# Performance work log

Measured on AMD Instinct MI355X. Metric: run time of the kernel, lower is better.

Reference implementation:

```python
import jax, jax.numpy as jnp
import numpy as np

DIM = 768
HEADS = 12
DIM_HEAD = DIM // HEADS  # 64
INNER = DIM_HEAD * HEADS  # 768
HIDDEN = 4 * DIM  # 3072
N = 31  # num_patches + 1, fixed by Block (num_patches=30)
B = 512
EPS = 1e-5
MASK_VAL = -987654321.0


def layernorm(x, g, b):
    mu = jnp.mean(x, axis=-1, keepdims=True)
    var = jnp.mean(jnp.square(x - mu), axis=-1, keepdims=True)
    return (x - mu) * jax.lax.rsqrt(var + EPS) * g + b


def setup_inputs() -> dict:
    key = jax.random.key(0)
    ks = jax.random.split(key, 12)
    s = 0.02
    return {
        "x": jax.random.normal(ks[0], (B, N, DIM), jnp.float32),
        "ln1_g": jnp.ones((DIM,), jnp.float32),
        "ln1_b": jnp.zeros((DIM,), jnp.float32),
        "w_qkv": jax.random.normal(ks[1], (DIM, 3 * INNER), jnp.float32) * s,
        "scale": jnp.full((HEADS,), DIM_HEAD ** -0.5, jnp.float32),
        "w_o": jax.random.normal(ks[2], (INNER, DIM), jnp.float32) * s,
        "b_o": jnp.zeros((DIM,), jnp.float32),
        "ln2_g": jnp.ones((DIM,), jnp.float32),
        "ln2_b": jnp.zeros((DIM,), jnp.float32),
        "w1": jax.random.normal(ks[3], (DIM, HIDDEN), jnp.float32) * s,
        "b1": jnp.zeros((HIDDEN,), jnp.float32),
        "w2": jax.random.normal(ks[4], (HIDDEN, DIM), jnp.float32) * s,
        "b2": jnp.zeros((DIM,), jnp.float32),
    }


def reference(x, ln1_g, ln1_b, w_qkv, scale, w_o, b_o, ln2_g, ln2_b, w1, b1, w2, b2):
    b, n, _ = x.shape
    # --- LSA attention ---
    h = layernorm(x, ln1_g, ln1_b)
    qkv = h @ w_qkv  # [b, n, 3*inner]
    q, k, v = jnp.split(qkv, 3, axis=-1)
    def split_heads(t):
        return t.reshape(b, n, HEADS, DIM_HEAD).transpose(0, 2, 1, 3)  # b h n d
    q, k, v = split_heads(q), split_heads(k), split_heads(v)
    dots = jnp.einsum('bhid,bhjd->bhij', q, k) * scale[None, :, None, None]
    # diagonal exclusion mask (self-token masked out)
    diag = jnp.eye(n, dtype=bool)
    dots = jnp.where(diag[None, None], MASK_VAL, dots)
    attn = jax.nn.softmax(dots, axis=-1)
    out = jnp.einsum('bhij,bhjd->bhid', attn, v)
    out = out.transpose(0, 2, 1, 3).reshape(b, n, INNER)
    x = x + out @ w_o + b_o
    # --- MLP ---
    h2 = layernorm(x, ln2_g, ln2_b)
    h2 = jax.nn.gelu(h2 @ w1 + b1, approximate=False)
    x = x + h2 @ w2 + b2
    return x
```

## Files before the change

### kernel.cpp

```cpp
#include <hip/hip_runtime.h>
#include <math.h>

#define DIM 768
#define HEADS 12
#define DHEAD 64
#define NTOK 31
#define BATCH 512
#define MTOK (BATCH * NTOK)
#define HIDDEN 3072
#define QKVN 2304
#define MASK_VAL -987654321.0f

typedef short s16x8 __attribute__((ext_vector_type(8)));
typedef float f32x4 __attribute__((ext_vector_type(4)));

static __device__ __forceinline__ float bs2f(unsigned short u) {
  unsigned int x = ((unsigned int)u) << 16;
  return __builtin_bit_cast(float, x);
}
static __device__ __forceinline__ unsigned short f2bs(float f) {
  unsigned int x = __builtin_bit_cast(unsigned int, f);
  x += 0x7fffu + ((x >> 16) & 1u);
  return (unsigned short)(x >> 16);
}

static __device__ __forceinline__ void gload16(const unsigned short* g, unsigned short* l) {
  __builtin_amdgcn_global_load_lds(
      (const __attribute__((address_space(1))) unsigned int*)g,
      (__attribute__((address_space(3))) unsigned int*)l, 16, 0, 0);
}

static __device__ __forceinline__ float epi_apply(int EPI, float v, int col, size_t idx,
                                                  const float* bias, const void* resid) {
  if (EPI == 0) return v;
  if (EPI == 2) {
    float t = v + bias[col];
    float arg = 1.5957691216f * t * (1.f + 0.044715f * t * t);
    return t * __builtin_amdgcn_rcpf(1.f + __expf(-arg));
  }
  if (EPI == 3) return v + bias[col] + ((const float*)resid)[idx];
  return v + bias[col] + bs2f(((const unsigned short*)resid)[idx]);
}

static __device__ __forceinline__ void epi_store(int EPI, void* outp, size_t idx, float t) {
  if (EPI == 4) ((float*)outp)[idx] = t;
  else ((unsigned short*)outp)[idx] = f2bs(t);
}

__global__ __launch_bounds__(256) void transpose_kernel(const float* __restrict__ w,
                                                        unsigned short* __restrict__ wt,
                                                        int K, int N) {
  __shared__ float t[64][65];
  int k0 = blockIdx.y * 64, n0 = blockIdx.x * 64;
  int tid = threadIdx.x;
  int r = tid >> 4, c4 = (tid & 15) * 4;
#pragma unroll
  for (int i = 0; i < 4; ++i) {
    float4 v = *(const float4*)(w + (size_t)(k0 + r + i * 16) * N + n0 + c4);
    t[r + i * 16][c4] = v.x;
    t[r + i * 16][c4 + 1] = v.y;
    t[r + i * 16][c4 + 2] = v.z;
    t[r + i * 16][c4 + 3] = v.w;
  }
  __syncthreads();
#pragma unroll
  for (int i = 0; i < 4; ++i) {
    int n = r + i * 16;
    ushort4 o;
    o.x = f2bs(t[c4 + 0][n]);
    o.y = f2bs(t[c4 + 1][n]);
    o.z = f2bs(t[c4 + 2][n]);
    o.w = f2bs(t[c4 + 3][n]);
    *(ushort4*)(wt + (size_t)(n0 + n) * K + k0 + c4) = o;
  }
}

__global__ __launch_bounds__(256) void ln_kernel(const float* __restrict__ x,
                                                 const float* __restrict__ g,
                                                 const float* __restrict__ bta,
                                                 unsigned short* __restrict__ out) {
  int wid = threadIdx.x >> 6, lane = threadIdx.x & 63;
  size_t row = (size_t)blockIdx.x * 4 + wid;
  const float4* xr = (const float4*)(x + row * DIM);
  float4 v[3];
  v[0] = xr[lane];
  v[1] = xr[lane + 64];
  v[2] = xr[lane + 128];
  float s = 0.f, sq = 0.f;
#pragma unroll
  for (int i = 0; i < 3; ++i) {
    s += v[i].x + v[i].y + v[i].z + v[i].w;
    sq += v[i].x * v[i].x + v[i].y * v[i].y + v[i].z * v[i].z + v[i].w * v[i].w;
  }
#pragma unroll
  for (int off = 32; off; off >>= 1) {
    s += __shfl_xor(s, off);
    sq += __shfl_xor(sq, off);
  }
  float mu = s * (1.f / DIM);
  float var = sq * (1.f / DIM) - mu * mu;
  float rs = rsqrtf(var + 1e-5f);
#pragma unroll
  for (int i = 0; i < 3; ++i) {
    int col = i * 256 + lane * 4;
    float4 gg = *(const float4*)(g + col);
    float4 bb = *(const float4*)(bta + col);
    ushort4 o;
    o.x = f2bs((v[i].x - mu) * rs * gg.x + bb.x);
    o.y = f2bs((v[i].y - mu) * rs * gg.y + bb.y);
    o.z = f2bs((v[i].z - mu) * rs * gg.z + bb.z);
    o.w = f2bs((v[i].w - mu) * rs * gg.w + bb.w);
    *(ushort4*)(out + row * DIM + col) = o;
  }
}

__global__ __launch_bounds__(256) void ln_bf16_kernel(const unsigned short* __restrict__ x,
                                                      const float* __restrict__ g,
                                                      const float* __restrict__ bta,
                                                      unsigned short* __restrict__ out) {
  int wid = threadIdx.x >> 6, lane = threadIdx.x & 63;
  size_t row = (size_t)blockIdx.x * 4 + wid;
  const unsigned short* xr = x + row * DIM;
  float v[12];
#pragma unroll
  for (int i = 0; i < 3; ++i) {
    ushort4 u = *(const ushort4*)(xr + i * 256 + lane * 4);
    v[i * 4 + 0] = bs2f(u.x);
    v[i * 4 + 1] = bs2f(u.y);
    v[i * 4 + 2] = bs2f(u.z);
    v[i * 4 + 3] = bs2f(u.w);
  }
  float s = 0.f, sq = 0.f;
#pragma unroll
  for (int i = 0; i < 12; ++i) {
    s += v[i];
    sq += v[i] * v[i];
  }
#pragma unroll
  for (int off = 32; off; off >>= 1) {
    s += __shfl_xor(s, off);
    sq += __shfl_xor(sq, off);
  }
  float mu = s * (1.f / DIM);
  float var = sq * (1.f / DIM) - mu * mu;
  float rs = rsqrtf(var + 1e-5f);
#pragma unroll
  for (int i = 0; i < 3; ++i) {
    int col = i * 256 + lane * 4;
    float4 gg = *(const float4*)(g + col);
    float4 bb = *(const float4*)(bta + col);
    ushort4 o;
    o.x = f2bs((v[i * 4 + 0] - mu) * rs * gg.x + bb.x);
    o.y = f2bs((v[i * 4 + 1] - mu) * rs * gg.y + bb.y);
    o.z = f2bs((v[i * 4 + 2] - mu) * rs * gg.z + bb.z);
    o.w = f2bs((v[i * 4 + 3] - mu) * rs * gg.w + bb.w);
    *(ushort4*)(out + row * DIM + col) = o;
  }
}

template <int BUF, int MH, int KH, int VM, typename STF>
__device__ __forceinline__ void gphase(const char* aP0, const char* aP1,
                                       const char* bP0, const char* bP1,
                                       s16x8* bk, f32x4 (&acc)[8][4], STF&& stage) {
  const char* aP = BUF ? aP1 : aP0;
  const char* bP = BUF ? bP1 : bP0;
  s16x8 af[4];
  if (MH == 0) {
#pragma unroll
    for (int ni = 0; ni < 4; ++ni)
      bk[ni] = *(const s16x8*)(bP + KH * 16384 + ni * 1024);
  }
#pragma unroll
  for (int mi = 0; mi < 4; ++mi)
    af[mi] = *(const s16x8*)(aP + KH * 16384 + MH * 4096 + mi * 1024);
  stage();
  if (VM == 10) asm volatile("s_waitcnt vmcnt(10)");
  if (VM == 4) asm volatile("s_waitcnt vmcnt(4)");
  if (VM == 0) asm volatile("s_waitcnt vmcnt(0)");
  __builtin_amdgcn_s_barrier();
  asm volatile("s_waitcnt lgkmcnt(0)");
  __builtin_amdgcn_s_setprio(1);
#pragma unroll
  for (int mi = 0; mi < 4; ++mi)
#pragma unroll
    for (int ni = 0; ni < 4; ++ni)
      acc[MH * 4 + mi][ni] =
          __builtin_amdgcn_mfma_f32_16x16x32_bf16(af[mi], bk[ni], acc[MH * 4 + mi][ni], 0, 0, 0);
  __builtin_amdgcn_s_setprio(0);
  __builtin_amdgcn_s_barrier();
}

template <int EPI>
__device__ __forceinline__ void gemm8_body(
    const unsigned short* __restrict__ A, const unsigned short* __restrict__ Bt,
    void* __restrict__ outp, const float* __restrict__ bias,
    const void* __restrict__ resid, int M, int N, int K, int ntn) {
  __shared__ unsigned short lds[65536];
  const char* ldsb = (const char*)lds;
  int tid = threadIdx.x;
  int lane = tid & 63, w = tid >> 6;
  int wm = w >> 2, wn = w & 3;
  int fr = lane & 15, q = lane >> 4;

  int nwg = gridDim.x, orig = blockIdx.x;
  int qd = nwg >> 3, r8 = nwg & 7, xcd = orig & 7, loc = orig >> 3;
  int bid = (xcd < r8 ? xcd * (qd + 1) : r8 * (qd + 1) + (xcd - r8) * qd) + loc;
  int m0 = (bid / ntn) * 256, n0 = (bid % ntn) * 256;

  int rdoff = (q * 16) ^ (((fr >> 1) & 3) << 4);
  const char* aP0 = ldsb + (wm * 128 + fr) * 64 + rdoff;
  const char* aP1 = aP0 + 65536;
  const char* bP0 = ldsb + 32768 + (wn * 64 + fr) * 64 + rdoff;
  const char* bP1 = bP0 + 65536;

  int srow = tid >> 2;
  int seoff = (((tid & 3) ^ ((srow >> 1) & 3))) << 3;
  const char* Ab = (const char*)A + ((size_t)(m0 + srow) * K + seoff) * 2;
  const char* Bb = (const char*)Bt + ((size_t)(n0 + srow) * K + seoff) * 2;
  size_t rstep = (size_t)K * 256;

  auto stg = [&](int mat, int kh, int buf, int tile) {
    const char* gp = (mat ? Bb : Ab) + tile * 128 + kh * 64;
    unsigned short* lp = lds + buf * 32768 + mat * 16384 + kh * 8192 + w * 512;
    gload16((const unsigned short*)gp, lp);
    gload16((const unsigned short*)(gp + rstep), lp + 4096);
  };
  auto nop = [&] {};

  f32x4 acc[8][4] = {};
  s16x8 bk[4];
  int NT = K / 64;

  stg(1, 0, 0, 0);
  stg(0, 0, 0, 0);
  stg(1, 1, 0, 0);
  stg(0, 1, 0, 0);
  stg(1, 0, 1, 1);
  stg(0, 0, 1, 1);
  stg(1, 1, 1, 1);
  asm volatile("s_waitcnt vmcnt(6)");
  __builtin_amdgcn_s_barrier();

  for (int t = 0; t + 3 < NT; t += 2) {
    gphase<0, 0, 0, -1>(aP0, aP1, bP0, bP1, bk, acc, [&] { stg(0, 1, 1, t + 1); });
    gphase<0, 1, 0, 10>(aP0, aP1, bP0, bP1, bk, acc, [&] { stg(1, 0, 0, t + 2); });
    gphase<0, 0, 1, -1>(aP0, aP1, bP0, bP1, bk, acc, [&] { stg(0, 0, 0, t + 2); });
    gphase<0, 1, 1, 10>(aP0, aP1, bP0, bP1, bk, acc, [&] { stg(1, 1, 0, t + 2); });
    gphase<1, 0, 0, -1>(aP0, aP1, bP0, bP1, bk, acc, [&] { stg(0, 1, 0, t + 2); });
    gphase<1, 1, 0, 10>(aP0, aP1, bP0, bP1, bk, acc, [&] { stg(1, 0, 1, t + 3); });
    gphase<1, 0, 1, -1>(aP0, aP1, bP0, bP1, bk, acc, [&] { stg(0, 0, 1, t + 3); });
    gphase<1, 1, 1, 10>(aP0, aP1, bP0, bP1, bk, acc, [&] { stg(1, 1, 1, t + 3); });
  }
  gphase<0, 0, 0, -1>(aP0, aP1, bP0, bP1, bk, acc, [&] { stg(0, 1, 1, NT - 1); });
  gphase<0, 1, 0, -1>(aP0, aP1, bP0, bP1, bk, acc, nop);
  gphase<0, 0, 1, -1>(aP0, aP1, bP0, bP1, bk, acc, nop);
  gphase<0, 1, 1, 4>(aP0, aP1, bP0, bP1, bk, acc, nop);
  gphase<1, 0, 0, -1>(aP0, aP1, bP0, bP1, bk, acc, nop);
  gphase<1, 1, 0, 0>(aP0, aP1, bP0, bP1, bk, acc, nop);
  gphase<1, 0, 1, -1>(aP0, aP1, bP0, bP1, bk, acc, nop);
  gphase<1, 1, 1, -1>(aP0, aP1, bP0, bP1, bk, acc, nop);

#pragma unroll
  for (int am = 0; am < 8; ++am)
#pragma unroll
    for (int ni = 0; ni < 4; ++ni)
#pragma unroll
      for (int rr = 0; rr < 4; ++rr) {
        int row = m0 + wm * 128 + am * 16 + (lane >> 4) * 4 + rr;
        int col = n0 + wn * 64 + ni * 16 + fr;
        size_t idx = (size_t)row * N + col;
        epi_store(EPI, outp, idx, epi_apply(EPI, acc[am][ni][rr], col, idx, bias, resid));
      }
}

template <int BUF, int MH, int KH, int VM, typename STF>
__device__ __forceinline__ void gph192(const char* aB0, const char* bKH0, const char* bKH1,
                                       s16x8 (&bk)[3], f32x4 (&acc)[8][3], STF&& stage) {
  const char* aP = aB0 + BUF * 32768 + KH * 16384 + MH * 4096;
  s16x8 af[4];
  if (MH == 0) {
    const char* bp = (KH ? bKH1 : bKH0) + BUF * 24576;
#pragma unroll
    for (int ni = 0; ni < 3; ++ni) bk[ni] = *(const s16x8*)(bp + ni * 2048);
  }
#pragma unroll
  for (int mi = 0; mi < 4; ++mi) af[mi] = *(const s16x8*)(aP + mi * 1024);
  stage();
  if (VM == 2) asm volatile("s_waitcnt vmcnt(2)");
  if (VM == 0) asm volatile("s_waitcnt vmcnt(0)");
  __builtin_amdgcn_s_barrier();
  asm volatile("s_waitcnt lgkmcnt(0)");
  __builtin_amdgcn_s_setprio(1);
#pragma unroll
  for (int mi = 0; mi < 4; ++mi)
#pragma unroll
    for (int ni = 0; ni < 3; ++ni)
      acc[MH * 4 + mi][ni] =
          __builtin_amdgcn_mfma_f32_16x16x32_bf16(af[mi], bk[ni], acc[MH * 4 + mi][ni], 0, 0, 0);
  __builtin_amdgcn_s_setprio(0);
  __builtin_amdgcn_s_barrier();
}

template <int EPI>
__device__ __forceinline__ void gemm192_body(
    const unsigned short* __restrict__ A, const unsigned short* __restrict__ Bt,
    void* __restrict__ outp, const float* __restrict__ bias,
    const void* __restrict__ resid, int M, int N, int K, int ntn) {
  __shared__ char ldsc[114688];
  int tid = threadIdx.x;
  int lane = tid & 63, w = tid >> 6;
  int wm = w >> 2, wn = w & 3;
  int fr = lane & 15, q = lane >> 4;

  int nwg = gridDim.x, orig = blockIdx.x;
  int qd = nwg >> 3, r8 = nwg & 7, xcd = orig & 7, loc = orig >> 3;
  int bid = (xcd < r8 ? xcd * (qd + 1) : r8 * (qd + 1) + (xcd - r8) * qd) + loc;
  int m0 = (bid / ntn) * 256, n0 = (bid % ntn) * 192;

  int rdoffA = (q * 16) ^ (((fr >> 1) & 3) << 4);
  const char* aB0 = ldsc + (wm * 128 + fr) * 64 + rdoffA;
  int brow0 = wn * 48 + fr;
  int bsw = brow0 & 7;
  const char* bBase = ldsc + 65536 + brow0 * 128 + (q ^ (bsw & 3)) * 16;
  const char* bKH0 = bBase + ((0 ^ (bsw >> 2)) * 64);
  const char* bKH1 = bBase + ((1 ^ (bsw >> 2)) * 64);

  int srow = tid >> 2;
  int seoffA = (((tid & 3) ^ ((srow >> 1) & 3))) << 3;
  const char* Ab = (const char*)A + ((size_t)(m0 + srow) * K + seoffA) * 2;
  size_t rstep = (size_t)K * 256;
  auto stgA = [&](int kh, int buf, int tile) {
    const char* gp = Ab + tile * 128 + kh * 64;
    unsigned short* lp = (unsigned short*)(ldsc + buf * 32768 + kh * 16384 + w * 1024);
    gload16((const unsigned short*)gp, lp);
    gload16((const unsigned short*)(gp + rstep), (unsigned short*)((char*)lp + 8192));
  };
  const char* Bb2 = (const char*)Bt +
                    ((size_t)(n0 + (tid >> 3)) * K + (((tid & 7) ^ ((tid >> 3) & 7)) * 8)) * 2;
  auto stgB = [&](int j, int buf, int tile) {
    gload16((const unsigned short*)(Bb2 + (size_t)j * 128 * K + tile * 128),
            (unsigned short*)(ldsc + 65536 + buf * 24576 + j * 8192 + w * 1024));
  };
  auto nop = [&] {};

  f32x4 acc[8][3] = {};
  s16x8 bk[3];
  int NT = K / 64;

  stgA(0, 0, 0);
  stgA(1, 0, 0);
  stgB(0, 0, 0);
  stgB(1, 0, 0);
  stgB(2, 0, 0);
  stgA(0, 1, 1);
  asm volatile("s_waitcnt vmcnt(2)");
  __builtin_amdgcn_s_barrier();

  for (int t = 0; t + 3 < NT; t += 2) {
    gph192<0, 0, 0, -1>(aB0, bKH0, bKH1, bk, acc,
                        [&] { stgA(1, 1, t + 1); stgB(0, 1, t + 1); stgB(1, 1, t + 1); });
    gph192<0, 1, 0, -1>(aB0, bKH0, bKH1, bk, acc, [&] { stgB(2, 1, t + 1); });
    gph192<0, 0, 1, -1>(aB0, bKH0, bKH1, bk, acc, [&] { stgA(0, 0, t + 2); });
    gph192<0, 1, 1, 2>(aB0, bKH0, bKH1, bk, acc, nop);
    gph192<1, 0, 0, -1>(aB0, bKH0, bKH1, bk, acc,
                        [&] { stgA(1, 0, t + 2); stgB(0, 0, t + 2); stgB(1, 0, t + 2); });
    gph192<1, 1, 0, -1>(aB0, bKH0, bKH1, bk, acc, [&] { stgB(2, 0, t + 2); });
    gph192<1, 0, 1, -1>(aB0, bKH0, bKH1, bk, acc, [&] { stgA(0, 1, t + 3); });
    gph192<1, 1, 1, 2>(aB0, bKH0, bKH1, bk, acc, nop);
  }
  gph192<0, 0, 0, -1>(aB0, bKH0, bKH1, bk, acc,
                      [&] { stgA(1, 1, NT - 1); stgB(0, 1, NT - 1); stgB(1, 1, NT - 1); });
  gph192<0, 1, 0, -1>(aB0, bKH0, bKH1, bk, acc, [&] { stgB(2, 1, NT - 1); });
  gph192<0, 0, 1, -1>(aB0, bKH0, bKH1, bk, acc, nop);
  gph192<0, 1, 1, 0>(aB0, bKH0, bKH1, bk, acc, nop);
  gph192<1, 0, 0, -1>(aB0, bKH0, bKH1, bk, acc, nop);
  gph192<1, 1, 0, -1>(aB0, bKH0, bKH1, bk, acc, nop);
  gph192<1, 0, 1, -1>(aB0, bKH0, bKH1, bk, acc, nop);
  gph192<1, 1, 1, -1>(aB0, bKH0, bKH1, bk, acc, nop);

#pragma unroll
  for (int am = 0; am < 8; ++am)
#pragma unroll
    for (int ni = 0; ni < 3; ++ni)
#pragma unroll
      for (int rr = 0; rr < 4; ++rr) {
        int row = m0 + wm * 128 + am * 16 + q * 4 + rr;
        int col = n0 + wn * 48 + ni * 16 + fr;
        size_t idx = (size_t)row * N + col;
        epi_store(EPI, outp, idx, epi_apply(EPI, acc[am][ni][rr], col, idx, bias, resid));
      }
}

__global__ __launch_bounds__(512, 2) void gemm_qkv(const unsigned short* A,
                                                   const unsigned short* Bt, void* o,
                                                   const float* b, const void* r, int M,
                                                   int N, int K, int ntn) {
  gemm8_body<0>(A, Bt, o, b, r, M, N, K, ntn);
}
__global__ __launch_bounds__(512, 2) void gemm_mlp1(const unsigned short* A,
                                                    const unsigned short* Bt, void* o,
                                                    const float* b, const void* r, int M,
                                                    int N, int K, int ntn) {
  gemm8_body<2>(A, Bt, o, b, r, M, N, K, ntn);
}
__global__ __launch_bounds__(512, 2) void gemm_proj(const unsigned short* A,
                                                    const unsigned short* Bt, void* o,
                                                    const float* b, const void* r, int M,
                                                    int N, int K, int ntn) {
  gemm192_body<3>(A, Bt, o, b, r, M, N, K, ntn);
}
__global__ __launch_bounds__(512, 2) void gemm_mlp2(const unsigned short* A,
                                                    const unsigned short* Bt, void* o,
                                                    const float* b, const void* r, int M,
                                                    int N, int K, int ntn) {
  gemm192_body<4>(A, Bt, o, b, r, M, N, K, ntn);
}

__global__ __launch_bounds__(256) void attn_mfma_kernel(const unsigned short* __restrict__ qkv,
                                                        const float* __restrict__ scale,
                                                        unsigned short* __restrict__ ao) {
  __shared__ unsigned short Vt[4][64][40];
  __shared__ unsigned short Pl[4][32][32];
  int wid = threadIdx.x >> 6, lane = threadIdx.x & 63;
  int pair = blockIdx.x * 4 + wid;
  int b = pair / HEADS, h = pair % HEADS;
  const unsigned short* base = qkv + (size_t)b * NTOK * QKVN + h * DHEAD;
  const unsigned short* Qp = base;
  const unsigned short* Kp = base + 768;
  const unsigned short* Vp = base + 1536;

  int c = lane & 15, q = lane >> 4;
  int oct = q * 8;

  unsigned short vcol[NTOK];
#pragma unroll
  for (int j = 0; j < NTOK; ++j) vcol[j] = Vp[(size_t)j * QKVN + lane];
#pragma unroll
  for (int j = 0; j < NTOK; ++j) Vt[wid][lane][j] = vcol[j];
  Vt[wid][lane][31] = 0;

  s16x8 kf[2][2] = {{{0}}}, qf[2][2] = {{{0}}};
#pragma unroll
  for (int t = 0; t < 2; ++t) {
    int row = t * 16 + c;
    if (row < NTOK) {
#pragma unroll
      for (int s = 0; s < 2; ++s) {
        kf[t][s] = *(const s16x8*)(Kp + (size_t)row * QKVN + s * 32 + oct);
        qf[t][s] = *(const s16x8*)(Qp + (size_t)row * QKVN + s * 32 + oct);
      }
    }
  }

  f32x4 st[2][2] = {};
#pragma unroll
  for (int jt = 0; jt < 2; ++jt)
#pragma unroll
    for (int it = 0; it < 2; ++it)
#pragma unroll
      for (int s = 0; s < 2; ++s)
        st[jt][it] =
            __builtin_amdgcn_mfma_f32_16x16x32_bf16(kf[jt][s], qf[it][s], st[jt][it], 0, 0, 0);

  float scl = scale[h];
  float p[2][2][4];
#pragma unroll
  for (int it = 0; it < 2; ++it)
#pragma unroll
    for (int jt = 0; jt < 2; ++jt)
#pragma unroll
      for (int r = 0; r < 4; ++r) {
        int j = jt * 16 + 4 * q + r;
        int i = it * 16 + c;
        float v = st[jt][it][r] * scl;
        if (j == 31 || j == i) v = MASK_VAL;
        p[it][jt][r] = v;
      }
#pragma unroll
  for (int it = 0; it < 2; ++it) {
    float m = p[it][0][0];
#pragma unroll
    for (int jt = 0; jt < 2; ++jt)
#pragma unroll
      for (int r = 0; r < 4; ++r) m = fmaxf(m, p[it][jt][r]);
    m = fmaxf(m, __shfl_xor(m, 16));
    m = fmaxf(m, __shfl_xor(m, 32));
    float s = 0.f;
#pragma unroll
    for (int jt = 0; jt < 2; ++jt)
#pragma unroll
      for (int r = 0; r < 4; ++r) {
        float e = __expf(p[it][jt][r] - m);
        p[it][jt][r] = e;
        s += e;
      }
    s += __shfl_xor(s, 16);
    s += __shfl_xor(s, 32);
    float inv = __builtin_amdgcn_rcpf(s);
#pragma unroll
    for (int jt = 0; jt < 2; ++jt)
#pragma unroll
      for (int r = 0; r < 4; ++r) p[it][jt][r] *= inv;
  }
#pragma unroll
  for (int it = 0; it < 2; ++it)
#pragma unroll
    for (int jt = 0; jt < 2; ++jt) {
      unsigned int w0 =
          (unsigned int)f2bs(p[it][jt][0]) | ((unsigned int)f2bs(p[it][jt][1]) << 16);
      unsigned int w1 =
          (unsigned int)f2bs(p[it][jt][2]) | ((unsigned int)f2bs(p[it][jt][3]) << 16);
      uint2 pk = {w0, w1};
      *(uint2*)&Pl[wid][it * 16 + c][jt * 16 + 4 * q] = pk;
    }

  s16x8 pa[2];
#pragma unroll
  for (int it = 0; it < 2; ++it) pa[it] = *(const s16x8*)&Pl[wid][it * 16 + c][oct];
  f32x4 o[2][4];
#pragma unroll
  for (int it = 0; it < 2; ++it)
#pragma unroll
    for (int dt = 0; dt < 4; ++dt) {
      s16x8 vb = *(const s16x8*)&Vt[wid][dt * 16 + c][oct];
      f32x4 z = {0.f, 0.f, 0.f, 0.f};
      o[it][dt] = __builtin_amdgcn_mfma_f32_16x16x32_bf16(pa[it], vb, z, 0, 0, 0);
    }
#pragma unroll
  for (int it = 0; it < 2; ++it)
#pragma unroll
    for (int r = 0; r < 4; ++r) {
      int i = it * 16 + 4 * q + r;
      if (i < NTOK) {
        size_t rowoff = ((size_t)b * NTOK + i) * DIM + h * DHEAD;
#pragma unroll
        for (int dt = 0; dt < 4; ++dt) ao[rowoff + dt * 16 + c] = f2bs(o[it][dt][r]);
      }
    }
}

extern "C" void kernel_launch(void* const* d_in, const int* in_sizes, int n_in,
                              void* d_out, int out_size, void* d_ws, size_t ws_size,
                              hipStream_t stream) {
  (void)in_sizes; (void)n_in; (void)out_size; (void)ws_size;
  const float* x = (const float*)d_in[0];
  const float* ln1_g = (const float*)d_in[1];
  const float* ln1_b = (const float*)d_in[2];
  const float* w_qkv = (const float*)d_in[3];
  const float* scale = (const float*)d_in[4];
  const float* w_o = (const float*)d_in[5];
  const float* b_o = (const float*)d_in[6];
  const float* ln2_g = (const float*)d_in[7];
  const float* ln2_b = (const float*)d_in[8];
  const float* w1 = (const float*)d_in[9];
  const float* b1 = (const float*)d_in[10];
  const float* w2 = (const float*)d_in[11];
  const float* b2 = (const float*)d_in[12];

  char* ws = (char*)d_ws;
  unsigned short* buf1 = (unsigned short*)(ws + 0);
  unsigned short* qkv_bf = (unsigned short*)(ws + 24379392);
  unsigned short* x2 = (unsigned short*)(ws + 24379392);
  unsigned short* g_bf = (unsigned short*)(ws + 97517568);
  unsigned short* wqkvT = (unsigned short*)(ws + 195035136);
  unsigned short* woT = (unsigned short*)(ws + 198574080);
  unsigned short* w1T = (unsigned short*)(ws + 199753728);
  unsigned short* w2T = (unsigned short*)(ws + 204472320);

  transpose_kernel<<<dim3(QKVN / 64, DIM / 64), 256, 0, stream>>>(w_qkv, wqkvT, DIM, QKVN);
  transpose_kernel<<<dim3(DIM / 64, DIM / 64), 256, 0, stream>>>(w_o, woT, DIM, DIM);
  transpose_kernel<<<dim3(HIDDEN / 64, DIM / 64), 256, 0, stream>>>(w1, w1T, DIM, HIDDEN);
  transpose_kernel<<<dim3(DIM / 64, HIDDEN / 64), 256, 0, stream>>>(w2, w2T, HIDDEN, DIM);

  ln_kernel<<<MTOK / 4, 256, 0, stream>>>(x, ln1_g, ln1_b, buf1);
  gemm_qkv<<<(MTOK / 256) * (QKVN / 256), 512, 0, stream>>>(
      buf1, wqkvT, qkv_bf, nullptr, nullptr, MTOK, QKVN, DIM, QKVN / 256);
  attn_mfma_kernel<<<(BATCH * HEADS) / 4, 256, 0, stream>>>(qkv_bf, scale, buf1);
  gemm_proj<<<(MTOK / 256) * (DIM / 192), 512, 0, stream>>>(
      buf1, woT, x2, b_o, x, MTOK, DIM, DIM, DIM / 192);
  ln_bf16_kernel<<<MTOK / 4, 256, 0, stream>>>(x2, ln2_g, ln2_b, buf1);
  gemm_mlp1<<<(MTOK / 256) * (HIDDEN / 256), 512, 0, stream>>>(
      buf1, w1T, g_bf, b1, nullptr, MTOK, HIDDEN, DIM, HIDDEN / 256);
  gemm_mlp2<<<(MTOK / 256) * (DIM / 192), 512, 0, stream>>>(
      g_bf, w2T, (float*)d_out, b2, x2, MTOK, DIM, HIDDEN, DIM / 192);
}
```

Before: 330.3 us.

## Shrink QKV and MLP1 GEMM tiles to 128x256 with K-step 32

Replaces the 256x256 GEMM body used by the QKV and MLP1 projections with a 128x256 tile, a 32-wide K step and 48KB of LDS. The pipeline staging, wait counts and launch bounds (now 4 blocks per CU hint) are reworked to match, and the grids double in M. The intent is more workgroups and higher occupancy to cut tail effects and raise latency hiding, at the cost of less operand reuse per tile and more barriers per unit of K.

Result: faster. 322.7 us (-2.3%).

```diff
diff --git a/kernel.cpp b/kernel.cpp
--- a/kernel.cpp
+++ b/kernel.cpp
@@ -158,45 +158,40 @@
   }
 }
 
-template <int BUF, int MH, int KH, int VM, typename STF>
-__device__ __forceinline__ void gphase(const char* aP0, const char* aP1,
-                                       const char* bP0, const char* bP1,
-                                       s16x8* bk, f32x4 (&acc)[8][4], STF&& stage) {
-  const char* aP = BUF ? aP1 : aP0;
-  const char* bP = BUF ? bP1 : bP0;
-  s16x8 af[4];
+template <int BUF, int MH, int VM, typename STF>
+__device__ __forceinline__ void gph128(const char* aP0, const char* bP0,
+                                       s16x8 (&bk)[4], f32x4 (&acc)[4][4], STF&& stage) {
+  const char* aP = aP0 + BUF * 8192 + MH * 2048;
+  const char* bP = bP0 + BUF * 16384;
+  s16x8 af[2];
   if (MH == 0) {
 #pragma unroll
-    for (int ni = 0; ni < 4; ++ni)
-      bk[ni] = *(const s16x8*)(bP + KH * 16384 + ni * 1024);
-  }
-#pragma unroll
-  for (int mi = 0; mi < 4; ++mi)
-    af[mi] = *(const s16x8*)(aP + KH * 16384 + MH * 4096 + mi * 1024);
+    for (int ni = 0; ni < 4; ++ni) bk[ni] = *(const s16x8*)(bP + ni * 1024);
+  }
+  af[0] = *(const s16x8*)(aP);
+  af[1] = *(const s16x8*)(aP + 1024);
   stage();
-  if (VM == 10) asm volatile("s_waitcnt vmcnt(10)");
-  if (VM == 4) asm volatile("s_waitcnt vmcnt(4)");
+  if (VM == 2) asm volatile("s_waitcnt vmcnt(2)");
   if (VM == 0) asm volatile("s_waitcnt vmcnt(0)");
   __builtin_amdgcn_s_barrier();
   asm volatile("s_waitcnt lgkmcnt(0)");
   __builtin_amdgcn_s_setprio(1);
 #pragma unroll
-  for (int mi = 0; mi < 4; ++mi)
+  for (int mi = 0; mi < 2; ++mi)
 #pragma unroll
     for (int ni = 0; ni < 4; ++ni)
-      acc[MH * 4 + mi][ni] =
-          __builtin_amdgcn_mfma_f32_16x16x32_bf16(af[mi], bk[ni], acc[MH * 4 + mi][ni], 0, 0, 0);
+      acc[MH * 2 + mi][ni] =
+          __builtin_amdgcn_mfma_f32_16x16x32_bf16(af[mi], bk[ni], acc[MH * 2 + mi][ni], 0, 0, 0);
   __builtin_amdgcn_s_setprio(0);
   __builtin_amdgcn_s_barrier();
 }
 
 template <int EPI>
-__device__ __forceinline__ void gemm8_body(
+__device__ __forceinline__ void gemm128_body(
     const unsigned short* __restrict__ A, const unsigned short* __restrict__ Bt,
     void* __restrict__ outp, const float* __restrict__ bias,
     const void* __restrict__ resid, int M, int N, int K, int ntn) {
-  __shared__ unsigned short lds[65536];
-  const char* ldsb = (const char*)lds;
+  __shared__ char ldsc[49152];
   int tid = threadIdx.x;
   int lane = tid & 63, w = tid >> 6;
   int wm = w >> 2, wn = w & 3;
@@ -205,13 +200,11 @@
   int nwg = gridDim.x, orig = blockIdx.x;
   int qd = nwg >> 3, r8 = nwg & 7, xcd = orig & 7, loc = orig >> 3;
   int bid = (xcd < r8 ? xcd * (qd + 1) : r8 * (qd + 1) + (xcd - r8) * qd) + loc;
-  int m0 = (bid / ntn) * 256, n0 = (bid % ntn) * 256;
+  int m0 = (bid / ntn) * 128, n0 = (bid % ntn) * 256;
 
   int rdoff = (q * 16) ^ (((fr >> 1) & 3) << 4);
-  const char* aP0 = ldsb + (wm * 128 + fr) * 64 + rdoff;
-  const char* aP1 = aP0 + 65536;
-  const char* bP0 = ldsb + 32768 + (wn * 64 + fr) * 64 + rdoff;
-  const char* bP1 = bP0 + 65536;
+  const char* aP0 = ldsc + (wm * 64 + fr) * 64 + rdoff;
+  const char* bP0 = ldsc + 16384 + (wn * 64 + fr) * 64 + rdoff;
 
   int srow = tid >> 2;
   int seoff = (((tid & 3) ^ ((srow >> 1) & 3))) << 3;
@@ -219,54 +212,46 @@
   const char* Bb = (const char*)Bt + ((size_t)(n0 + srow) * K + seoff) * 2;
   size_t rstep = (size_t)K * 256;
 
-  auto stg = [&](int mat, int kh, int buf, int tile) {
-    const char* gp = (mat ? Bb : Ab) + tile * 128 + kh * 64;
-    unsigned short* lp = lds + buf * 32768 + mat * 16384 + kh * 8192 + w * 512;
-    gload16((const unsigned short*)gp, lp);
-    gload16((const unsigned short*)(gp + rstep), lp + 4096);
+  auto stgA = [&](int buf, int tile) {
+    gload16((const unsigned short*)(Ab + tile * 64),
+            (unsigned short*)(ldsc + buf * 8192 + w * 1024));
+  };
+  auto stgB = [&](int buf, int tile) {
+    const char* gp = Bb + tile * 64;
+    char* lp = ldsc + 16384 + buf * 16384 + w * 1024;
+    gload16((const unsigned short*)gp, (unsigned short*)lp);
+    gload16((const unsigned short*)(gp + rstep), (unsigned short*)(lp + 8192));
   };
   auto nop = [&] {};
 
-  f32x4 acc[8][4] = {};
+  f32x4 acc[4][4] = {};
   s16x8 bk[4];
-  int NT = K / 64;
-
-  stg(1, 0, 0, 0);
-  stg(0, 0, 0, 0);
-  stg(1, 1, 0, 0);
-  stg(0, 1, 0, 0);
-  stg(1, 0, 1, 1);
-  stg(0, 0, 1, 1);
-  stg(1, 1, 1, 1);
-  asm volatile("s_waitcnt vmcnt(6)");
+  int NT = K / 32;
+
+  stgA(0, 0);
+  stgB(0, 0);
+  stgB(1, 1);
+  asm volatile("s_waitcnt vmcnt(2)");
   __builtin_amdgcn_s_barrier();
 
   for (int t = 0; t + 3 < NT; t += 2) {
-    gphase<0, 0, 0, -1>(aP0, aP1, bP0, bP1, bk, acc, [&] { stg(0, 1, 1, t + 1); });
-    gphase<0, 1, 0, 10>(aP0, aP1, bP0, bP1, bk, acc, [&] { stg(1, 0, 0, t + 2); });
-    gphase<0, 0, 1, -1>(aP0, aP1, bP0, bP1, bk, acc, [&] { stg(0, 0, 0, t + 2); });
-    gphase<0, 1, 1, 10>(aP0, aP1, bP0, bP1, bk, acc, [&] { stg(1, 1, 0, t + 2); });
-    gphase<1, 0, 0, -1>(aP0, aP1, bP0, bP1, bk, acc, [&] { stg(0, 1, 0, t + 2); });
-    gphase<1, 1, 0, 10>(aP0, aP1, bP0, bP1, bk, acc, [&] { stg(1, 0, 1, t + 3); });
-    gphase<1, 0, 1, -1>(aP0, aP1, bP0, bP1, bk, acc, [&] { stg(0, 0, 1, t + 3); });
-    gphase<1, 1, 1, 10>(aP0, aP1, bP0, bP1, bk, acc, [&] { stg(1, 1, 1, t + 3); });
-  }
-  gphase<0, 0, 0, -1>(aP0, aP1, bP0, bP1, bk, acc, [&] { stg(0, 1, 1, NT - 1); });
-  gphase<0, 1, 0, -1>(aP0, aP1, bP0, bP1, bk, acc, nop);
-  gphase<0, 0, 1, -1>(aP0, aP1, bP0, bP1, bk, acc, nop);
-  gphase<0, 1, 1, 4>(aP0, aP1, bP0, bP1, bk, acc, nop);
-  gphase<1, 0, 0, -1>(aP0, aP1, bP0, bP1, bk, acc, nop);
-  gphase<1, 1, 0, 0>(aP0, aP1, bP0, bP1, bk, acc, nop);
-  gphase<1, 0, 1, -1>(aP0, aP1, bP0, bP1, bk, acc, nop);
-  gphase<1, 1, 1, -1>(aP0, aP1, bP0, bP1, bk, acc, nop);
-
-#pragma unroll
-  for (int am = 0; am < 8; ++am)
+    gph128<0, 0, -1>(aP0, bP0, bk, acc, [&] { stgA(1, t + 1); });
+    gph128<0, 1, 2>(aP0, bP0, bk, acc, [&] { stgB(0, t + 2); });
+    gph128<1, 0, -1>(aP0, bP0, bk, acc, [&] { stgA(0, t + 2); });
+    gph128<1, 1, 2>(aP0, bP0, bk, acc, [&] { stgB(1, t + 3); });
+  }
+  gph128<0, 0, -1>(aP0, bP0, bk, acc, [&] { stgA(1, NT - 1); });
+  gph128<0, 1, 0>(aP0, bP0, bk, acc, nop);
+  gph128<1, 0, -1>(aP0, bP0, bk, acc, nop);
+  gph128<1, 1, -1>(aP0, bP0, bk, acc, nop);
+
+#pragma unroll
+  for (int am = 0; am < 4; ++am)
 #pragma unroll
     for (int ni = 0; ni < 4; ++ni)
 #pragma unroll
       for (int rr = 0; rr < 4; ++rr) {
-        int row = m0 + wm * 128 + am * 16 + (lane >> 4) * 4 + rr;
+        int row = m0 + wm * 64 + am * 16 + q * 4 + rr;
         int col = n0 + wn * 64 + ni * 16 + fr;
         size_t idx = (size_t)row * N + col;
         epi_store(EPI, outp, idx, epi_apply(EPI, acc[am][ni][rr], col, idx, bias, resid));
@@ -391,17 +376,17 @@
       }
 }
 
-__global__ __launch_bounds__(512, 2) void gemm_qkv(const unsigned short* A,
+__global__ __launch_bounds__(512, 4) void gemm_qkv(const unsigned short* A,
                                                    const unsigned short* Bt, void* o,
                                                    const float* b, const void* r, int M,
                                                    int N, int K, int ntn) {
-  gemm8_body<0>(A, Bt, o, b, r, M, N, K, ntn);
-}
-__global__ __launch_bounds__(512, 2) void gemm_mlp1(const unsigned short* A,
+  gemm128_body<0>(A, Bt, o, b, r, M, N, K, ntn);
+}
+__global__ __launch_bounds__(512, 4) void gemm_mlp1(const unsigned short* A,
                                                     const unsigned short* Bt, void* o,
                                                     const float* b, const void* r, int M,
                                                     int N, int K, int ntn) {
-  gemm8_body<2>(A, Bt, o, b, r, M, N, K, ntn);
+  gemm128_body<2>(A, Bt, o, b, r, M, N, K, ntn);
 }
 __global__ __launch_bounds__(512, 2) void gemm_proj(const unsigned short* A,
                                                     const unsigned short* Bt, void* o,
@@ -573,13 +558,13 @@
   transpose_kernel<<<dim3(DIM / 64, HIDDEN / 64), 256, 0, stream>>>(w2, w2T, HIDDEN, DIM);
 
   ln_kernel<<<MTOK / 4, 256, 0, stream>>>(x, ln1_g, ln1_b, buf1);
-  gemm_qkv<<<(MTOK / 256) * (QKVN / 256), 512, 0, stream>>>(
+  gemm_qkv<<<(MTOK / 128) * (QKVN / 256), 512, 0, stream>>>(
       buf1, wqkvT, qkv_bf, nullptr, nullptr, MTOK, QKVN, DIM, QKVN / 256);
   attn_mfma_kernel<<<(BATCH * HEADS) / 4, 256, 0, stream>>>(qkv_bf, scale, buf1);
   gemm_proj<<<(MTOK / 256) * (DIM / 192), 512, 0, stream>>>(
       buf1, woT, x2, b_o, x, MTOK, DIM, DIM, DIM / 192);
   ln_bf16_kernel<<<MTOK / 4, 256, 0, stream>>>(x2, ln2_g, ln2_b, buf1);
-  gemm_mlp1<<<(MTOK / 256) * (HIDDEN / 256), 512, 0, stream>>>(
+  gemm_mlp1<<<(MTOK / 128) * (HIDDEN / 256), 512, 0, stream>>>(
       buf1, w1T, g_bf, b1, nullptr, MTOK, HIDDEN, DIM, HIDDEN / 256);
   gemm_mlp2<<<(MTOK / 256) * (DIM / 192), 512, 0, stream>>>(
       g_bf, w2T, (float*)d_out, b2, x2, MTOK, DIM, HIDDEN, DIM / 192);
```
